# Optimization experiments

Measured on AMD Instinct MI355X. Metric: run time of the kernel, lower is better.

Reference implementation:

```python
import jax, jax.numpy as jnp
import numpy as np

N_EMBD = 1024
HEAD_SIZE = 64
B, T = 8, 2048


def setup_inputs() -> dict:
    key = jax.random.key(0)
    k1, k2, k3, k4 = jax.random.split(key, 4)
    scale = 1.0 / np.sqrt(N_EMBD)
    return {
        "x": jax.random.normal(k1, (B, T, N_EMBD), dtype=jnp.float32),
        "Wq": jax.random.normal(k2, (N_EMBD, HEAD_SIZE), dtype=jnp.float32) * scale,
        "Wk": jax.random.normal(k3, (N_EMBD, HEAD_SIZE), dtype=jnp.float32) * scale,
        "Wv": jax.random.normal(k4, (N_EMBD, HEAD_SIZE), dtype=jnp.float32) * scale,
    }


def reference(x, Wq, Wk, Wv):
    # x: [B, T, C]; projections (no bias)
    q = jnp.einsum("btc,ch->bth", x, Wq)
    k = jnp.einsum("btc,ch->bth", x, Wk)
    v = jnp.einsum("btc,ch->bth", x, Wv)
    head_size = k.shape[-1]
    # scaled scores [B, T, T]
    wei = jnp.einsum("bth,bsh->bts", q, k) * (head_size ** -0.5)
    # causal mask (lower-triangular keeps)
    Tlen = x.shape[1]
    causal = jnp.tril(jnp.ones((Tlen, Tlen), dtype=bool))
    wei = jnp.where(causal[None, :, :], wei, -jnp.inf)
    wei = jax.nn.softmax(wei, axis=-1)
    # dropout p=0 (eval) -> identity
    out = jnp.einsum("bts,bsh->bth", wei, v)
    return out
```

## Files before the change

kernel.cpp:

```cpp
#include <hip/hip_runtime.h>
#include <hip/hip_bf16.h>
#include <math.h>

#define Bn 8
#define Tn 2048
#define Cn 1024
#define Hn 64

typedef __attribute__((ext_vector_type(8))) short short8;
typedef __attribute__((ext_vector_type(4))) float floatx4;
typedef __attribute__((ext_vector_type(4))) _Float16 half4;

#define ATTN_SCALE 0.18033688011112042f

__device__ inline unsigned short f2bf(float f) {
    union { float f; unsigned int u; } x; x.f = f;
    unsigned int r = x.u + 0x7fffu + ((x.u >> 16) & 1u);
    return (unsigned short)(r >> 16);
}

__device__ inline uint2 pack4bf(float4 v) {
    __hip_bfloat162 lo = __float22bfloat162_rn(make_float2(v.x, v.y));
    __hip_bfloat162 hi = __float22bfloat162_rn(make_float2(v.z, v.w));
    uint2 r;
    r.x = *reinterpret_cast<unsigned int*>(&lo);
    r.y = *reinterpret_cast<unsigned int*>(&hi);
    return r;
}

__global__ __launch_bounds__(256) void prep_w(
    const float* __restrict__ Wq, const float* __restrict__ Wk,
    const float* __restrict__ Wv, unsigned short* __restrict__ Wfrag)
{
    const int gid = blockIdx.x * 256 + threadIdx.x;
    const int c    = gid >> 11;
    const int rem  = gid & 2047;
    const int ks   = rem >> 6;
    const int lane = rem & 63;
    const int ln = lane & 15, qd = lane >> 4;
    const int mat = c >> 2, nc = c & 3;
    const float* W = (mat == 0) ? Wq : (mat == 1) ? Wk : Wv;
    const float sc = (mat == 0) ? ATTN_SCALE : 1.0f;
    const int col = nc * 16 + ln;
    unsigned short o[8];
    #pragma unroll
    for (int j = 0; j < 8; ++j)
        o[j] = f2bf(W[(size_t)(ks * 32 + qd * 8 + j) * Hn + col] * sc);
    *reinterpret_cast<short8*>(Wfrag + (size_t)gid * 8) = *reinterpret_cast<short8*>(o);
}

__global__ __launch_bounds__(256, 4) void proj_mfma(
    const float* __restrict__ x, const unsigned short* __restrict__ Wfrag,
    unsigned short* __restrict__ qbf, unsigned short* __restrict__ kfrag,
    unsigned short* __restrict__ vfrag)
{
    __shared__ unsigned short xs[32 * 512];

    const int ln   = threadIdx.x & 15;
    const int quad = (threadIdx.x >> 4) & 3;
    const int w    = threadIdx.x >> 6;
    const int lane = threadIdx.x & 63;
    const int row0 = blockIdx.x * 16;

    const int srow = threadIdx.x >> 4;
    const int sf   = threadIdx.x & 15;
    const float4* xrow4 = reinterpret_cast<const float4*>(x + (size_t)(row0 + srow) * Cn);

    float4 ld[16];
    #pragma unroll
    for (int it = 0; it < 16; ++it)
        ld[it] = xrow4[sf + 16 * it];
    #pragma unroll
    for (int it = 0; it < 16; ++it) {
        const int f4g = sf + 16 * it;
        const int s = f4g >> 3;
        const int q = (f4g >> 1) & 3;
        const int j = (f4g & 1) * 4;
        *reinterpret_cast<uint2*>(&xs[s * 512 + (q * 16 + srow) * 8 + j]) = pack4bf(ld[it]);
    }
    __syncthreads();

    floatx4 acc[3];
    #pragma unroll
    for (int i = 0; i < 3; ++i) acc[i] = (floatx4){0.f, 0.f, 0.f, 0.f};

    #pragma unroll 4
    for (int s = 0; s < 32; ++s) {
        const short8 a = *reinterpret_cast<const short8*>(&xs[s * 512 + lane * 8]);
        #pragma unroll
        for (int i = 0; i < 3; ++i) {
            const int cc = w * 3 + i;
            const short8 b = *reinterpret_cast<const short8*>(
                Wfrag + ((size_t)(cc * 32 + s) * 64 + lane) * 8);
            acc[i] = __builtin_amdgcn_mfma_f32_16x16x32_bf16(a, b, acc[i], 0, 0, 0);
        }
    }

    const int t0   = row0 + quad * 4;
    const int b    = t0 >> 11;
    const int tloc = t0 & 2047;
    #pragma unroll
    for (int i = 0; i < 3; ++i) {
        const int idx = w * 3 + i;
        const int mat = idx >> 2, ch = idx & 3;
        if (mat == 0) {
            #pragma unroll
            for (int r = 0; r < 4; ++r)
                qbf[(size_t)(t0 + r) * Hn + ch * 16 + ln] = f2bf(acc[i][r]);
        } else if (mat == 1) {
            const int kc = tloc >> 4;
            const int ks = ch >> 1;
            const int lq = (ch & 1) * 2 + (ln >> 3);
            #pragma unroll
            for (int r = 0; r < 4; ++r) {
                const int lanep = (quad * 4 + r) + 16 * lq;
                kfrag[(((size_t)(b * 128 + kc) * 2 + ks) * 64 + lanep) * 8 + (ln & 7)]
                    = f2bf(acc[i][r]);
            }
        } else {
            const int t16 = tloc >> 4;
            union { _Float16 h[4]; ushort4 u; } cv;
            cv.h[0] = (_Float16)acc[i][0]; cv.h[1] = (_Float16)acc[i][1];
            cv.h[2] = (_Float16)acc[i][2]; cv.h[3] = (_Float16)acc[i][3];
            *reinterpret_cast<ushort4*>(
                vfrag + (((size_t)(b * 128 + t16) * 4 + ch) * 64 + ln + 16 * quad) * 4) = cv.u;
        }
    }
}

__global__ __launch_bounds__(256, 4) void attn_mfma(
    const unsigned short* __restrict__ qbf, const unsigned short* __restrict__ kfrag,
    const unsigned short* __restrict__ vfrag, float* __restrict__ out)
{
    __shared__ float o_lds[4][16][68];
    __shared__ float l_lds[4][16];

    const int j  = blockIdx.x;
    const int b  = j & 7;
    const int ti = 127 - (j >> 3);
    const int q0 = ti * 16;

    const int ln   = threadIdx.x & 15;
    const int quad = (threadIdx.x >> 4) & 3;
    const int w    = threadIdx.x >> 6;
    const int lane = threadIdx.x & 63;

    const unsigned short* qb = qbf + (size_t)b * Tn * Hn;
    const unsigned short* Kb = kfrag + (size_t)b * 131072;
    const unsigned short* Vb = vfrag + (size_t)b * 131072;

    const short8 aq0 = *reinterpret_cast<const short8*>(qb + (size_t)(q0 + ln) * Hn + quad * 8);
    const short8 aq1 = *reinterpret_cast<const short8*>(qb + (size_t)(q0 + ln) * Hn + 32 + quad * 8);

    floatx4 O[4];
    #pragma unroll
    for (int c = 0; c < 4; ++c) O[c] = (floatx4){0.f, 0.f, 0.f, 0.f};
    float lp = 0.f;

    const int ntiles = ti + 1;
    const int per    = (ntiles + 3) >> 2;
    const int beg    = w * per;
    const int end    = min(beg + per, ntiles);

    union U4 { ushort4 u; half4 h; };
    short8 kf0, kf1; U4 vf[4];
    if (beg < end) {
        kf0 = *reinterpret_cast<const short8*>(Kb + (size_t)(beg * 2) * 512 + lane * 8);
        kf1 = *reinterpret_cast<const short8*>(Kb + (size_t)(beg * 2 + 1) * 512 + lane * 8);
        #pragma unroll
        for (int c = 0; c < 4; ++c)
            vf[c].u = *reinterpret_cast<const ushort4*>(Vb + (size_t)(beg * 4 + c) * 256 + lane * 4);
    }

    for (int t = beg; t < end; ++t) {
        const int tn = (t + 1 < end) ? (t + 1) : t;
        short8 kn0, kn1; U4 vn[4];
        kn0 = *reinterpret_cast<const short8*>(Kb + (size_t)(tn * 2) * 512 + lane * 8);
        kn1 = *reinterpret_cast<const short8*>(Kb + (size_t)(tn * 2 + 1) * 512 + lane * 8);
        #pragma unroll
        for (int c = 0; c < 4; ++c)
            vn[c].u = *reinterpret_cast<const ushort4*>(Vb + (size_t)(tn * 4 + c) * 256 + lane * 4);

        const floatx4 z = (floatx4){0.f, 0.f, 0.f, 0.f};
        floatx4 St = __builtin_amdgcn_mfma_f32_16x16x32_bf16(kf0, aq0, z, 0, 0, 0);
        St = __builtin_amdgcn_mfma_f32_16x16x32_bf16(kf1, aq1, St, 0, 0, 0);

        const bool diag = (t == ntiles - 1);
        half4 pa;
        #pragma unroll
        for (int r = 0; r < 4; ++r) {
            float sv = St[r];
            if (diag && (quad * 4 + r > ln)) sv = -1e30f;
            const float p = exp2f(sv);
            lp += p;
            pa[r] = (_Float16)p;
        }
        #pragma unroll
        for (int c = 0; c < 4; ++c)
            O[c] = __builtin_amdgcn_mfma_f32_16x16x16f16(pa, vf[c].h, O[c], 0, 0, 0);

        kf0 = kn0; kf1 = kn1;
        #pragma unroll
        for (int c = 0; c < 4; ++c) vf[c] = vn[c];
    }

    #pragma unroll
    for (int c = 0; c < 4; ++c)
        #pragma unroll
        for (int r = 0; r < 4; ++r)
            o_lds[w][quad * 4 + r][c * 16 + ln] = O[c][r];
    {
        float lt = lp;
        lt += __shfl_xor(lt, 16);
        lt += __shfl_xor(lt, 32);
        if (quad == 0) l_lds[w][ln] = lt;
    }
    __syncthreads();

    const int qq = threadIdx.x >> 4;
    const int dg = threadIdx.x & 15;
    const float ltot = l_lds[0][qq] + l_lds[1][qq] + l_lds[2][qq] + l_lds[3][qq];
    const float inv = 1.0f / ltot;
    const float4 a0 = *reinterpret_cast<float4*>(&o_lds[0][qq][dg * 4]);
    const float4 a1 = *reinterpret_cast<float4*>(&o_lds[1][qq][dg * 4]);
    const float4 a2 = *reinterpret_cast<float4*>(&o_lds[2][qq][dg * 4]);
    const float4 a3 = *reinterpret_cast<float4*>(&o_lds[3][qq][dg * 4]);
    float4 r;
    r.x = (a0.x + a1.x + a2.x + a3.x) * inv;
    r.y = (a0.y + a1.y + a2.y + a3.y) * inv;
    r.z = (a0.z + a1.z + a2.z + a3.z) * inv;
    r.w = (a0.w + a1.w + a2.w + a3.w) * inv;
    *reinterpret_cast<float4*>(out + ((size_t)b * Tn + q0 + qq) * Hn + dg * 4) = r;
}

extern "C" void kernel_launch(void* const* d_in, const int* in_sizes, int n_in,
                              void* d_out, int out_size, void* d_ws, size_t ws_size,
                              hipStream_t stream) {
    (void)in_sizes; (void)n_in; (void)out_size; (void)ws_size;
    const float* x  = (const float*)d_in[0];
    const float* Wq = (const float*)d_in[1];
    const float* Wk = (const float*)d_in[2];
    const float* Wv = (const float*)d_in[3];
    float* out = (float*)d_out;

    unsigned short* Wfrag = (unsigned short*)d_ws;
    unsigned short* qbf   = Wfrag + (size_t)196608;
    unsigned short* kfr   = qbf + (size_t)Bn * Tn * Hn;
    unsigned short* vfr   = kfr + (size_t)Bn * 131072;

    prep_w<<<96, 256, 0, stream>>>(Wq, Wk, Wv, Wfrag);
    proj_mfma<<<(Bn * Tn) / 16, 256, 0, stream>>>(x, Wfrag, qbf, kfr, vfr);
    attn_mfma<<<Bn * (Tn / 16), 256, 0, stream>>>(qbf, kfr, vfr, out);
}
```

Baseline: 129.3 us.

## Process 32-key tiles per iteration using 16x16x32 f16 MFMA for PV

Result: faster. 125.6 us (-2.8%).

```diff
diff --git a/kernel.cpp b/kernel.cpp
--- a/kernel.cpp
+++ b/kernel.cpp
@@ -9,7 +9,7 @@
 
 typedef __attribute__((ext_vector_type(8))) short short8;
 typedef __attribute__((ext_vector_type(4))) float floatx4;
-typedef __attribute__((ext_vector_type(4))) _Float16 half4;
+typedef __attribute__((ext_vector_type(8))) _Float16 half8;
 
 #define ATTN_SCALE 0.18033688011112042f
 
@@ -118,12 +118,14 @@
                     = f2bf(acc[i][r]);
             }
         } else {
-            const int t16 = tloc >> 4;
+            const int t32 = tloc >> 5;
+            const int h16 = (tloc >> 4) & 1;
             union { _Float16 h[4]; ushort4 u; } cv;
             cv.h[0] = (_Float16)acc[i][0]; cv.h[1] = (_Float16)acc[i][1];
             cv.h[2] = (_Float16)acc[i][2]; cv.h[3] = (_Float16)acc[i][3];
             *reinterpret_cast<ushort4*>(
-                vfrag + (((size_t)(b * 128 + t16) * 4 + ch) * 64 + ln + 16 * quad) * 4) = cv.u;
+                vfrag + (((size_t)(b * 64 + t32) * 4 + ch) * 64 + ln + 16 * quad) * 8
+                      + h16 * 4) = cv.u;
         }
     }
 }
@@ -157,51 +159,57 @@
     for (int c = 0; c < 4; ++c) O[c] = (floatx4){0.f, 0.f, 0.f, 0.f};
     float lp = 0.f;
 
-    const int ntiles = ti + 1;
+    const int ntiles = (q0 + 47) >> 5;
     const int per    = (ntiles + 3) >> 2;
     const int beg    = w * per;
     const int end    = min(beg + per, ntiles);
 
-    union U4 { ushort4 u; half4 h; };
-    short8 kf0, kf1; U4 vf[4];
+    short8 kf[4]; half8 vf[4];
     if (beg < end) {
-        kf0 = *reinterpret_cast<const short8*>(Kb + (size_t)(beg * 2) * 512 + lane * 8);
-        kf1 = *reinterpret_cast<const short8*>(Kb + (size_t)(beg * 2 + 1) * 512 + lane * 8);
-        #pragma unroll
-        for (int c = 0; c < 4; ++c)
-            vf[c].u = *reinterpret_cast<const ushort4*>(Vb + (size_t)(beg * 4 + c) * 256 + lane * 4);
+        #pragma unroll
+        for (int u = 0; u < 4; ++u) {
+            kf[u] = *reinterpret_cast<const short8*>(Kb + (size_t)(beg * 4 + u) * 512 + lane * 8);
+            vf[u] = *reinterpret_cast<const half8*>(Vb + (size_t)(beg * 4 + u) * 512 + lane * 8);
+        }
     }
 
     for (int t = beg; t < end; ++t) {
         const int tn = (t + 1 < end) ? (t + 1) : t;
-        short8 kn0, kn1; U4 vn[4];
-        kn0 = *reinterpret_cast<const short8*>(Kb + (size_t)(tn * 2) * 512 + lane * 8);
-        kn1 = *reinterpret_cast<const short8*>(Kb + (size_t)(tn * 2 + 1) * 512 + lane * 8);
+        short8 kn[4]; half8 vn[4];
+        #pragma unroll
+        for (int u = 0; u < 4; ++u) {
+            kn[u] = *reinterpret_cast<const short8*>(Kb + (size_t)(tn * 4 + u) * 512 + lane * 8);
+            vn[u] = *reinterpret_cast<const half8*>(Vb + (size_t)(tn * 4 + u) * 512 + lane * 8);
+        }
+
+        const floatx4 z = (floatx4){0.f, 0.f, 0.f, 0.f};
+        floatx4 St0 = __builtin_amdgcn_mfma_f32_16x16x32_bf16(kf[0], aq0, z, 0, 0, 0);
+        St0 = __builtin_amdgcn_mfma_f32_16x16x32_bf16(kf[1], aq1, St0, 0, 0, 0);
+        floatx4 St1 = __builtin_amdgcn_mfma_f32_16x16x32_bf16(kf[2], aq0, z, 0, 0, 0);
+        St1 = __builtin_amdgcn_mfma_f32_16x16x32_bf16(kf[3], aq1, St1, 0, 0, 0);
+
+        const bool diag = (t == ntiles - 1);
+        const int koff = t * 32 - q0;
+        half8 pa;
+        #pragma unroll
+        for (int r = 0; r < 4; ++r) {
+            float s0 = St0[r], s1 = St1[r];
+            if (diag) {
+                if (koff + quad * 4 + r > ln)      s0 = -1e30f;
+                if (koff + 16 + quad * 4 + r > ln) s1 = -1e30f;
+            }
+            const float p0 = exp2f(s0);
+            const float p1 = exp2f(s1);
+            lp += p0 + p1;
+            pa[r]     = (_Float16)p0;
+            pa[r + 4] = (_Float16)p1;
+        }
         #pragma unroll
         for (int c = 0; c < 4; ++c)
-            vn[c].u = *reinterpret_cast<const ushort4*>(Vb + (size_t)(tn * 4 + c) * 256 + lane * 4);
-
-        const floatx4 z = (floatx4){0.f, 0.f, 0.f, 0.f};
-        floatx4 St = __builtin_amdgcn_mfma_f32_16x16x32_bf16(kf0, aq0, z, 0, 0, 0);
-        St = __builtin_amdgcn_mfma_f32_16x16x32_bf16(kf1, aq1, St, 0, 0, 0);
-
-        const bool diag = (t == ntiles - 1);
-        half4 pa;
-        #pragma unroll
-        for (int r = 0; r < 4; ++r) {
-            float sv = St[r];
-            if (diag && (quad * 4 + r > ln)) sv = -1e30f;
-            const float p = exp2f(sv);
-            lp += p;
-            pa[r] = (_Float16)p;
-        }
-        #pragma unroll
-        for (int c = 0; c < 4; ++c)
-            O[c] = __builtin_amdgcn_mfma_f32_16x16x16f16(pa, vf[c].h, O[c], 0, 0, 0);
-
-        kf0 = kn0; kf1 = kn1;
-        #pragma unroll
-        for (int c = 0; c < 4; ++c) vf[c] = vn[c];
+            O[c] = __builtin_amdgcn_mfma_f32_16x16x32_f16(pa, vf[c], O[c], 0, 0, 0);
+
+        #pragma unroll
+        for (int u = 0; u < 4; ++u) { kf[u] = kn[u]; vf[u] = vn[u]; }
     }
 
     #pragma unroll
```
